# Optimization experiments

Measured on AMD Instinct MI355X. Metric: run time of the kernel, lower is better.

## Reference

```python
import jax, jax.numpy as jnp
import numpy as np

B, S, H = 2, 1024, 2048
NH, HD = 16, 128
PAST = 1024
ROPE_THETA = 10000.0


def _rope(q, k, theta=ROPE_THETA):
    # q, k: [B, S, NH, HD]; standard rotate-half RoPE over current positions 0..S-1
    s, d = q.shape[1], q.shape[3]
    inv_freq = 1.0 / (theta ** (jnp.arange(0, d, 2, dtype=jnp.float32) / d))  # [d/2]
    freqs = jnp.arange(s, dtype=jnp.float32)[:, None] * inv_freq[None, :]      # [S, d/2]
    emb = jnp.concatenate([freqs, freqs], axis=-1)                             # [S, d]
    cos = jnp.cos(emb)[None, :, None, :]
    sin = jnp.sin(emb)[None, :, None, :]

    def rot_half(x):
        x1, x2 = jnp.split(x, 2, axis=-1)
        return jnp.concatenate([-x2, x1], axis=-1)

    return q * cos + rot_half(q) * sin, k * cos + rot_half(k) * sin


def setup_inputs() -> dict:
    key = jax.random.key(0)
    ks = jax.random.split(key, 12)
    hidden_states = jax.random.normal(ks[0], (B, S, H), dtype=jnp.float32)
    past_key = jax.random.normal(ks[1], (B, NH, PAST, HD), dtype=jnp.float32)
    past_value = jax.random.normal(ks[2], (B, NH, PAST, HD), dtype=jnp.float32)
    # causal mask accounting for cache: 1.0 where masked (query i cannot see kv j > PAST+i)
    q_pos = PAST + jnp.arange(S)[:, None]
    kv_pos = jnp.arange(PAST + S)[None, :]
    mask = jnp.broadcast_to((kv_pos > q_pos).astype(jnp.float32)[None, None], (B, 1, S, PAST + S))
    sc = 1.0 / np.sqrt(H)
    Wq = jax.random.normal(ks[3], (H, NH * HD), dtype=jnp.float32) * sc
    Wk = jax.random.normal(ks[4], (H, NH * HD), dtype=jnp.float32) * sc
    Wv = jax.random.normal(ks[5], (H, NH * HD), dtype=jnp.float32) * sc
    Wo = jax.random.normal(ks[6], (NH * HD, H), dtype=jnp.float32) * (1.0 / np.sqrt(NH * HD))
    bq = jnp.zeros((NH * HD,), jnp.float32)
    bk = jnp.zeros((NH * HD,), jnp.float32)
    bv = jnp.zeros((NH * HD,), jnp.float32)
    bo = jnp.zeros((H,), jnp.float32)
    return {"hidden_states": hidden_states, "mask": mask, "past_key": past_key,
            "past_value": past_value, "Wq": Wq, "bq": bq, "Wk": Wk, "bk": bk,
            "Wv": Wv, "bv": bv, "Wo": Wo, "bo": bo}


def reference(hidden_states, mask, past_key, past_value, Wq, bq, Wk, bk, Wv, bv, Wo, bo):
    b, s, _ = hidden_states.shape
    scale = 1.0 / jnp.sqrt(jnp.float32(HD))
    q = (hidden_states @ Wq + bq).reshape(b, s, NH, HD)
    k = (hidden_states @ Wk + bk).reshape(b, s, NH, HD)
    v = (hidden_states @ Wv + bv).reshape(b, s, NH, HD)
    q, k = _rope(q, k)
    q, k, v = (jnp.transpose(x, (0, 2, 1, 3)) for x in (q, k, v))  # [B,NH,S,HD]
    k = jnp.concatenate([past_key, k], axis=2)    # [B,NH,S_total,HD]
    v = jnp.concatenate([past_value, v], axis=2)
    scores = jnp.einsum('bhqd,bhkd->bhqk', q, k) * scale
    scores = scores + mask * (-1e9)               # mask broadcasts over heads
    probs = jax.nn.softmax(scores, axis=-1).astype(jnp.float32)
    out = jnp.einsum('bhqk,bhkd->bhqd', probs, v)
    out = out.transpose(0, 2, 1, 3).reshape(b, s, NH * HD)
    return out @ Wo + bo, k, v
```

## Files before the change

### kernel.cpp

```cpp
#include <hip/hip_runtime.h>
#include <hip/hip_bf16.h>
#include <math.h>

#define NB 2
#define SEQ 1024
#define HDIM 2048
#define NHEADS 16
#define HDHEAD 128
#define PASTN 1024
#define STOT 2048
#define MROWS 2048

typedef __attribute__((ext_vector_type(4))) float f32x4;
typedef __attribute__((ext_vector_type(8))) __bf16 bf16x8;
typedef __attribute__((ext_vector_type(8))) unsigned short us8;
typedef __attribute__((ext_vector_type(4))) unsigned short us4;

__device__ __forceinline__ unsigned short f2bf(float f) {
    union { float f; unsigned int u; } v; v.f = f;
    unsigned int u = v.u;
    u += 0x7FFFu + ((u >> 16) & 1u);
    return (unsigned short)(u >> 16);
}
__device__ __forceinline__ bf16x8 as_bf(us8 u) { return __builtin_bit_cast(bf16x8, u); }

__device__ __forceinline__ void gl16(const unsigned short* g, unsigned short* l) {
    __builtin_amdgcn_global_load_lds(
        (const __attribute__((address_space(1))) void*)g,
        (__attribute__((address_space(3))) void*)l, 16, 0, 0);
}

#define OFF_CS  ((size_t)0)
#define OFF_HSB (OFF_CS  + (size_t)SEQ*64*8)
#define OFF_WT  (OFF_HSB + (size_t)MROWS*HDIM*2)
#define OFF_QBF (OFF_WT  + (size_t)4*HDIM*HDIM*2)
#define OFF_KC  (OFF_QBF + (size_t)NB*NHEADS*SEQ*HDHEAD*2)
#define OFF_VT  (OFF_KC  + (size_t)NB*NHEADS*STOT*HDHEAD*2)
#define OFF_ATT (OFF_VT  + (size_t)NB*NHEADS*HDHEAD*STOT*2)


__global__ void k_prep(const float* __restrict__ in, unsigned short* __restrict__ hsb,
                       const float* __restrict__ pk, float* __restrict__ outK,
                       unsigned short* __restrict__ Kc2, float2* __restrict__ csT,
                       const float* __restrict__ Wq, const float* __restrict__ Wk,
                       const float* __restrict__ Wv, const float* __restrict__ Wo,
                       unsigned short* __restrict__ WT,
                       const float* __restrict__ pv, float* __restrict__ outV,
                       unsigned short* __restrict__ Vt2) {
    __shared__ unsigned short tsh[64][65];
    const int bid = blockIdx.x, tid = threadIdx.x;
    if (bid < 4096) {
        const int i = (bid * 256 + tid) * 4;
        {
            f32x4 v = *(const f32x4*)(in + i);
            us4 o;
            o.x = f2bf(v.x); o.y = f2bf(v.y); o.z = f2bf(v.z); o.w = f2bf(v.w);
            *(us4*)(hsb + i) = o;
        }
        {
            size_t e = (size_t)i;
            size_t bh = e >> 17;
            int p = (int)((e >> 7) & 1023);
            int d0 = (int)(e & 127);
            f32x4 v = *(const f32x4*)(pk + e);
            *(f32x4*)(outK + e + (bh << 17)) = v;
            us4 u;
            u.x = f2bf(v.x); u.y = f2bf(v.y); u.z = f2bf(v.z); u.w = f2bf(v.w);
            const int kt = p >> 6, pr = p & 63;
            *(us4*)(Kc2 + ((bh * 32 + kt) << 13) + (size_t)pr * 128 + (d0 ^ ((p & 7) << 3))) = u;
        }
        if (bid < 256) {
            const int idx = bid * 256 + tid;
            const int s = idx >> 6, fi = idx & 63;
            float inv = 1.0f / powf(10000.0f, (float)fi / 64.0f);
            float a = (float)s * inv;
            csT[idx] = make_float2(cosf(a), sinf(a));
        }
    } else if (bid < 8192) {
        const int idx = bid - 4096;
        const int z = idx >> 10;
        const int rem = idx & 1023;
        const int n0 = (rem & 31) * 64, k0 = (rem >> 5) * 64;
        const float* W = (z == 0) ? Wq : (z == 1) ? Wk : (z == 2) ? Wv : Wo;
        unsigned short* out = WT + (size_t)z * HDIM * HDIM;
        const int tx = tid & 63, ty = tid >> 6;
        #pragma unroll
        for (int j = 0; j < 16; ++j) {
            const int kk = ty + j * 4;
            tsh[tx][kk] = f2bf(W[(size_t)(k0 + kk) * HDIM + n0 + tx]);
        }
        __syncthreads();
        #pragma unroll
        for (int j = 0; j < 16; ++j) {
            const int nn = ty + j * 4;
            out[(size_t)(n0 + nn) * HDIM + k0 + tx] = tsh[nn][tx];
        }
    } else {
        const int idx = bid - 8192;
        const int bh = idx >> 5;
        const int rem = idx & 31;
        const int p0 = (rem & 15) * 64, d0 = (rem >> 4) * 64;
        const int tx = tid & 63, ty = tid >> 6;
        const float* src = pv + ((size_t)bh * PASTN + p0) * HDHEAD + d0;
        float* dst = outV + ((size_t)bh * STOT + p0) * HDHEAD + d0;
        #pragma unroll
        for (int j = 0; j < 16; ++j) {
            const int pp = ty + j * 4;
            float v = src[(size_t)pp * HDHEAD + tx];
            dst[(size_t)pp * HDHEAD + tx] = v;
            tsh[tx][pp] = f2bf(v);
        }
        __syncthreads();
        unsigned short* vt = Vt2 + (((size_t)bh * 32 + (p0 >> 6)) << 13);
        #pragma unroll
        for (int j = 0; j < 16; ++j) {
            const int dd = ty + j * 4;
            const int d = d0 + dd;
            vt[(size_t)d * 64 + (tx ^ ((d & 7) << 3))] = tsh[dd][tx];
        }
    }
}

__global__ __launch_bounds__(512, 2) void k_gemm_qkv(
    const unsigned short* __restrict__ hsb, const unsigned short* __restrict__ WT,
    const float* __restrict__ bv,
    float* __restrict__ Cq, float* __restrict__ Ck, float* __restrict__ outV) {
    __shared__ __align__(16) unsigned short As[2][256 * 64];
    __shared__ __align__(16) unsigned short Bs[2][256 * 64];

    const int bid = blockIdx.x;
    const int swz = (bid & 7) * 24 + (bid >> 3);
    const int mb = swz & 7;
    const int nbz = swz >> 3;
    const int z = nbz >> 3;
    const int nb8 = nbz & 7;
    const int m0 = mb * 256;
    const int n0 = nb8 * 256;
    const unsigned short* Wz = WT + (size_t)z * HDIM * HDIM;

    const int t = threadIdx.x;
    const int lane = t & 63, wid = t >> 6;
    const int wr = wid >> 1, wc = wid & 1;
    const int c = lane & 15, g = lane >> 4;

    const int lrow8 = lane >> 3;
    const int lslot = (lane & 7) ^ lrow8;
    const unsigned short* aB = hsb + (size_t)(m0 + lrow8) * HDIM + lslot * 8;
    const unsigned short* bB = Wz + (size_t)(n0 + lrow8) * HDIM + lslot * 8;

    auto stage = [&](int kt, int pb) {
        const int k0s = kt * 64;
        #pragma unroll
        for (int j = 0; j < 4; ++j) {
            const int ch = wid * 4 + j;
            gl16(aB + (size_t)(ch * 8) * HDIM + k0s, &As[pb][ch * 512]);
            gl16(bB + (size_t)(ch * 8) * HDIM + k0s, &Bs[pb][ch * 512]);
        }
    };

    f32x4 acc[4][8] = {};
    const int NT = HDIM / 64;

    stage(0, 0);
    stage(1, 1);

#define MF(A_, B_, C_) __builtin_amdgcn_mfma_f32_16x16x32_bf16(A_, B_, C_, 0, 0, 0)
#define RDA(D0, D1, MI) { const int ar_ = wr * 64 + (MI) * 16 + c; const int sa_ = ar_ & 7; \
    D0 = as_bf(*(const us8*)&As[p][ar_ * 64 + ((g ^ sa_) << 3)]); \
    D1 = as_bf(*(const us8*)&As[p][ar_ * 64 + (((4 + g) ^ sa_) << 3)]); }
#define RDB0(NI) { const int br_ = wc * 128 + (NI) * 16 + c; const int sb_ = br_ & 7; \
    b0[NI] = as_bf(*(const us8*)&Bs[p][br_ * 64 + ((g ^ sb_) << 3)]); }
#define RDB1(NI) { const int br_ = wc * 128 + (NI) * 16 + c; const int sb_ = br_ & 7; \
    b1[NI] = as_bf(*(const us8*)&Bs[p][br_ * 64 + (((4 + g) ^ sb_) << 3)]); }

    for (int kt = 0; kt < NT; ++kt) {
        const int p = kt & 1;
        if (kt + 1 < NT) {
            asm volatile("s_waitcnt vmcnt(8)" ::: "memory");
        } else {
            asm volatile("s_waitcnt vmcnt(0)" ::: "memory");
        }
        __builtin_amdgcn_s_barrier();

        bf16x8 b0[8], b1[8];
        bf16x8 a0c, a1c, a0n, a1n;
        RDA(a0c, a1c, 0)
        RDB0(0) RDB0(1) RDB0(2) RDB0(3)
        __builtin_amdgcn_s_setprio(1);
        RDB0(4) acc[0][0] = MF(a0c, b0[0], acc[0][0]);
        RDB0(5) acc[0][1] = MF(a0c, b0[1], acc[0][1]);
        RDB0(6) acc[0][2] = MF(a0c, b0[2], acc[0][2]);
        RDB0(7) acc[0][3] = MF(a0c, b0[3], acc[0][3]);
        RDB1(0) acc[0][4] = MF(a0c, b0[4], acc[0][4]);
        RDB1(1) acc[0][5] = MF(a0c, b0[5], acc[0][5]);
        RDB1(2) acc[0][6] = MF(a0c, b0[6], acc[0][6]);
        RDB1(3) acc[0][7] = MF(a0c, b0[7], acc[0][7]);
        RDB1(4) acc[0][0] = MF(a1c, b1[0], acc[0][0]);
        RDB1(5) acc[0][1] = MF(a1c, b1[1], acc[0][1]);
        RDB1(6) acc[0][2] = MF(a1c, b1[2], acc[0][2]);
        RDB1(7) acc[0][3] = MF(a1c, b1[3], acc[0][3]);
        RDA(a0n, a1n, 1)
        acc[0][4] = MF(a1c, b1[4], acc[0][4]);
        acc[0][5] = MF(a1c, b1[5], acc[0][5]);
        acc[0][6] = MF(a1c, b1[6], acc[0][6]);
        acc[0][7] = MF(a1c, b1[7], acc[0][7]);
        acc[1][0] = MF(a0n, b0[0], acc[1][0]);
        acc[1][1] = MF(a0n, b0[1], acc[1][1]);
        acc[1][2] = MF(a0n, b0[2], acc[1][2]);
        acc[1][3] = MF(a0n, b0[3], acc[1][3]);
        acc[1][4] = MF(a0n, b0[4], acc[1][4]);
        acc[1][5] = MF(a0n, b0[5], acc[1][5]);
        acc[1][6] = MF(a0n, b0[6], acc[1][6]);
        acc[1][7] = MF(a0n, b0[7], acc[1][7]);
        RDA(a0c, a1c, 2)
        acc[1][0] = MF(a1n, b1[0], acc[1][0]);
        acc[1][1] = MF(a1n, b1[1], acc[1][1]);
        acc[1][2] = MF(a1n, b1[2], acc[1][2]);
        acc[1][3] = MF(a1n, b1[3], acc[1][3]);
        acc[1][4] = MF(a1n, b1[4], acc[1][4]);
        acc[1][5] = MF(a1n, b1[5], acc[1][5]);
        acc[1][6] = MF(a1n, b1[6], acc[1][6]);
        acc[1][7] = MF(a1n, b1[7], acc[1][7]);
        acc[2][0] = MF(a0c, b0[0], acc[2][0]);
        acc[2][1] = MF(a0c, b0[1], acc[2][1]);
        acc[2][2] = MF(a0c, b0[2], acc[2][2]);
        acc[2][3] = MF(a0c, b0[3], acc[2][3]);
        acc[2][4] = MF(a0c, b0[4], acc[2][4]);
        acc[2][5] = MF(a0c, b0[5], acc[2][5]);
        acc[2][6] = MF(a0c, b0[6], acc[2][6]);
        acc[2][7] = MF(a0c, b0[7], acc[2][7]);
        RDA(a0n, a1n, 3)
        acc[2][0] = MF(a1c, b1[0], acc[2][0]);
        acc[2][1] = MF(a1c, b1[1], acc[2][1]);
        acc[2][2] = MF(a1c, b1[2], acc[2][2]);
        acc[2][3] = MF(a1c, b1[3], acc[2][3]);
        acc[2][4] = MF(a1c, b1[4], acc[2][4]);
        acc[2][5] = MF(a1c, b1[5], acc[2][5]);
        acc[2][6] = MF(a1c, b1[6], acc[2][6]);
        acc[2][7] = MF(a1c, b1[7], acc[2][7]);
        acc[3][0] = MF(a0n, b0[0], acc[3][0]);
        acc[3][1] = MF(a0n, b0[1], acc[3][1]);
        acc[3][2] = MF(a0n, b0[2], acc[3][2]);
        acc[3][3] = MF(a0n, b0[3], acc[3][3]);
        acc[3][4] = MF(a0n, b0[4], acc[3][4]);
        acc[3][5] = MF(a0n, b0[5], acc[3][5]);
        acc[3][6] = MF(a0n, b0[6], acc[3][6]);
        acc[3][7] = MF(a0n, b0[7], acc[3][7]);
        acc[3][0] = MF(a1n, b1[0], acc[3][0]);
        acc[3][1] = MF(a1n, b1[1], acc[3][1]);
        acc[3][2] = MF(a1n, b1[2], acc[3][2]);
        acc[3][3] = MF(a1n, b1[3], acc[3][3]);
        acc[3][4] = MF(a1n, b1[4], acc[3][4]);
        acc[3][5] = MF(a1n, b1[5], acc[3][5]);
        acc[3][6] = MF(a1n, b1[6], acc[3][6]);
        acc[3][7] = MF(a1n, b1[7], acc[3][7]);
        __builtin_amdgcn_s_setprio(0);
        __builtin_amdgcn_s_barrier();
        if (kt + 2 < NT) stage(kt + 2, p);
    }
#undef MF
#undef RDA
#undef RDB0
#undef RDB1

    if (z < 2) {
        float* Cz = (z == 0) ? Cq : Ck;
        #pragma unroll
        for (int mi = 0; mi < 4; ++mi) {
            #pragma unroll
            for (int r = 0; r < 4; ++r) {
                const size_t row = (size_t)(m0 + wr * 64 + mi * 16 + g * 4 + r);
                #pragma unroll
                for (int ni = 0; ni < 8; ++ni)
                    Cz[row * HDIM + n0 + wc * 128 + ni * 16 + c] = acc[mi][ni][r];
            }
        }
    } else {
        const int h = nb8 * 2 + wc;
        const int b = m0 >> 10;
        const size_t bh2 = (size_t)(b * NHEADS + h);
        float bias8[8];
        #pragma unroll
        for (int ni = 0; ni < 8; ++ni) bias8[ni] = bv[n0 + wc * 128 + ni * 16 + c];
        #pragma unroll
        for (int mi = 0; mi < 4; ++mi) {
            #pragma unroll
            for (int r = 0; r < 4; ++r) {
                const int row = m0 + wr * 64 + mi * 16 + g * 4 + r;
                const int s = row & 1023;
                const int p = PASTN + s;
                #pragma unroll
                for (int ni = 0; ni < 8; ++ni)
                    outV[(bh2 * STOT + p) * HDHEAD + ni * 16 + c] = acc[mi][ni][r] + bias8[ni];
            }
        }
    }
}

__global__ __launch_bounds__(256) void k_post(
    const float* __restrict__ Cq, const float* __restrict__ Ck,
    const float* __restrict__ outV,
    const float* __restrict__ bq, const float* __restrict__ bk,
    const float2* __restrict__ csT,
    unsigned short* __restrict__ qbf, unsigned short* __restrict__ Kc2,
    unsigned short* __restrict__ Vt2, float* __restrict__ outK) {
    __shared__ unsigned short tv[128][80];
    const int stile = blockIdx.x;
    const int bh = blockIdx.y;
    const int b = bh >> 4, h = bh & 15;
    const int tid = threadIdx.x;
    const int dq = (tid & 15) * 4;
    const int sl0 = tid >> 4;
    const int s0 = stile * 64;
    const int ktv = 16 + stile;
    const float qscale = 0.08838834764831845f * 1.44269504088896f;
    unsigned short* kc = Kc2 + (((size_t)bh * 32 + ktv) << 13);
    unsigned short* vt = Vt2 + (((size_t)bh * 32 + ktv) << 13);

    float bql[4], bqh[4], bkl[4], bkh[4];
    #pragma unroll
    for (int i = 0; i < 4; ++i) {
        bql[i] = bq[h * 128 + dq + i];      bqh[i] = bq[h * 128 + 64 + dq + i];
        bkl[i] = bk[h * 128 + dq + i];      bkh[i] = bk[h * 128 + 64 + dq + i];
    }

    #pragma unroll
    for (int ps = 0; ps < 4; ++ps) {
        const int sl = sl0 + ps * 16;
        const int s = s0 + sl;
        const size_t row = (size_t)b * 1024 + s;
        const int p = PASTN + s;
        float2 cs4[4];
        #pragma unroll
        for (int i = 0; i < 4; ++i) cs4[i] = csT[s * 64 + dq + i];
        const int swzp = (sl & 7) << 3;
        {
            const f32x4 a = *(const f32x4*)&Cq[row * HDIM + h * 128 + dq];
            const f32x4 bb = *(const f32x4*)&Cq[row * HDIM + h * 128 + dq + 64];
            us4 lo, hi;
            #pragma unroll
            for (int i = 0; i < 4; ++i) {
                const float va = a[i] + bql[i];
                const float vb = bb[i] + bqh[i];
                lo[i] = f2bf((va * cs4[i].x - vb * cs4[i].y) * qscale);
                hi[i] = f2bf((vb * cs4[i].x + va * cs4[i].y) * qscale);
            }
            unsigned short* qrow = qbf + ((size_t)bh * SEQ + s) * HDHEAD;
            *(us4*)&qrow[dq] = lo;
            *(us4*)&qrow[dq + 64] = hi;
        }
        {
            const f32x4 a = *(const f32x4*)&Ck[row * HDIM + h * 128 + dq];
            const f32x4 bb = *(const f32x4*)&Ck[row * HDIM + h * 128 + dq + 64];
            f32x4 rl, rh;
            us4 lo, hi;
            #pragma unroll
            for (int i = 0; i < 4; ++i) {
                const float va = a[i] + bkl[i];
                const float vb = bb[i] + bkh[i];
                rl[i] = va * cs4[i].x - vb * cs4[i].y;
                rh[i] = vb * cs4[i].x + va * cs4[i].y;
                lo[i] = f2bf(rl[i]);
                hi[i] = f2bf(rh[i]);
            }
            float* krow = outK + ((size_t)bh * STOT + p) * HDHEAD;
            *(f32x4*)&krow[dq] = rl;
            *(f32x4*)&krow[dq + 64] = rh;
            *(us4*)&kc[(size_t)sl * 128 + (dq ^ swzp)] = lo;
            *(us4*)&kc[(size_t)sl * 128 + ((dq + 64) ^ swzp)] = hi;
        }
        {
            const f32x4 va = *(const f32x4*)&outV[((size_t)bh * STOT + p) * HDHEAD + dq];
            const f32x4 vb = *(const f32x4*)&outV[((size_t)bh * STOT + p) * HDHEAD + dq + 64];
            #pragma unroll
            for (int i = 0; i < 4; ++i) {
                tv[dq + i][sl] = f2bf(va[i]);
                tv[dq + 64 + i][sl] = f2bf(vb[i]);
            }
        }
    }
    __syncthreads();
    const int d = tid >> 1;
    const int ph = (tid & 1) * 32;
    const int swzd = (d & 7) << 3;
    #pragma unroll
    for (int i = 0; i < 8; ++i) {
        const int pp = ph + i * 4;
        us4 u;
        u.x = tv[d][pp]; u.y = tv[d][pp + 1]; u.z = tv[d][pp + 2]; u.w = tv[d][pp + 3];
        *(us4*)&vt[(size_t)d * 64 + (pp ^ swzd)] = u;
    }
}

__global__ __launch_bounds__(256) void k_attn(
    const unsigned short* __restrict__ qbf, const unsigned short* __restrict__ Kc2,
    const unsigned short* __restrict__ Vt2, unsigned short* __restrict__ attn) {
    __shared__ __align__(16) unsigned short Ks[2][64 * 128];
    __shared__ __align__(16) unsigned short Vs[128 * 64];
    __shared__ __align__(16) unsigned short P[4][16][72];
    const int bid = blockIdx.x;
    const int bh = bid & 31;
    const int qt = bid >> 5;
    const int b = bh >> 4, h = bh & 15;
    const int t = threadIdx.x, lane = t & 63, w = t >> 6;
    const int c = lane & 15, g = lane >> 4;
    const int q0 = qt * 64 + w * 16;
    const unsigned short* Qb = qbf + ((size_t)bh * SEQ + q0) * HDHEAD;
    const unsigned short* Kbase = Kc2 + ((size_t)bh << 18);
    const unsigned short* Vbase = Vt2 + ((size_t)bh << 18);

    bf16x8 qf[4];
    #pragma unroll
    for (int kf = 0; kf < 4; ++kf)
        qf[kf] = as_bf(*(const us8*)(Qb + (size_t)c * HDHEAD + kf * 32 + g * 8));

    #pragma unroll
    for (int j = 0; j < 4; ++j) {
        const int ch = w * 4 + j;
        gl16(Kbase + ch * 512 + lane * 8, &Ks[0][ch * 512]);
    }

    f32x4 o[8] = {};
    float mrow[4] = {-1e30f, -1e30f, -1e30f, -1e30f};
    float lrow[4] = {0.f, 0.f, 0.f, 0.f};
    const int nkt = 17 + qt;
    int cur = 0;
    for (int kt = 0; kt < nkt; ++kt) {
        asm volatile("s_waitcnt vmcnt(0)" ::: "memory");
        __builtin_amdgcn_s_barrier();
        const unsigned short* Vg = Vbase + ((size_t)kt << 13);
        #pragma unroll
        for (int j = 0; j < 4; ++j) {
            const int ch = w * 4 + j;
            gl16(Vg + ch * 512 + lane * 8, &Vs[ch * 512]);
        }
        if (kt + 1 < nkt) {
            const unsigned short* Kg = Kbase + ((size_t)(kt + 1) << 13);
            #pragma unroll
            for (int j = 0; j < 4; ++j) {
                const int ch = w * 4 + j;
                gl16(Kg + ch * 512 + lane * 8, &Ks[cur ^ 1][ch * 512]);
            }
        }
        f32x4 sa[4] = {};
        #pragma unroll
        for (int nf = 0; nf < 4; ++nf) {
            const int row = nf * 16 + c;
            const int swzr = (row & 7) << 3;
            #pragma unroll
            for (int kf = 0; kf < 4; ++kf) {
                bf16x8 kf8 = as_bf(*(const us8*)&Ks[cur][row * 128 + ((kf * 32 + g * 8) ^ swzr)]);
                sa[nf] = __builtin_amdgcn_mfma_f32_16x16x32_bf16(qf[kf], kf8, sa[nf], 0, 0, 0);
            }
        }
        const int k0 = kt * 64;
        if (k0 + 63 > PASTN + q0) {
            #pragma unroll
            for (int nf = 0; nf < 4; ++nf) {
                const int j = k0 + nf * 16 + c;
                #pragma unroll
                for (int r = 0; r < 4; ++r)
                    if (j > PASTN + q0 + g * 4 + r) sa[nf][r] = -1e30f;
            }
        }
        float pmax[4];
        #pragma unroll
        for (int r = 0; r < 4; ++r)
            pmax[r] = fmaxf(fmaxf(sa[0][r], sa[1][r]), fmaxf(sa[2][r], sa[3][r]));
        bool need = false;
        #pragma unroll
        for (int r = 0; r < 4; ++r) need = need || (pmax[r] > mrow[r] + 12.0f);
        if (__any(need)) {
            #pragma unroll
            for (int r = 0; r < 4; ++r) {
                float mx = pmax[r];
                mx = fmaxf(mx, __shfl_xor(mx, 1));
                mx = fmaxf(mx, __shfl_xor(mx, 2));
                mx = fmaxf(mx, __shfl_xor(mx, 4));
                mx = fmaxf(mx, __shfl_xor(mx, 8));
                const float mnew = fmaxf(mrow[r], mx);
                const float alpha = exp2f(mrow[r] - mnew);
                mrow[r] = mnew;
                lrow[r] *= alpha;
                #pragma unroll
                for (int nd = 0; nd < 8; ++nd) o[nd][r] *= alpha;
            }
        }
        #pragma unroll
        for (int r = 0; r < 4; ++r) {
            const float p0 = exp2f(sa[0][r] - mrow[r]);
            const float p1 = exp2f(sa[1][r] - mrow[r]);
            const float p2 = exp2f(sa[2][r] - mrow[r]);
            const float p3 = exp2f(sa[3][r] - mrow[r]);
            lrow[r] += (p0 + p1) + (p2 + p3);
            P[w][g * 4 + r][0 * 16 + c] = f2bf(p0);
            P[w][g * 4 + r][1 * 16 + c] = f2bf(p1);
            P[w][g * 4 + r][2 * 16 + c] = f2bf(p2);
            P[w][g * 4 + r][3 * 16 + c] = f2bf(p3);
        }
        if (kt + 1 < nkt) {
            asm volatile("s_waitcnt vmcnt(4)" ::: "memory");
        } else {
            asm volatile("s_waitcnt vmcnt(0)" ::: "memory");
        }
        __builtin_amdgcn_s_barrier();
        #pragma unroll
        for (int kf2 = 0; kf2 < 2; ++kf2) {
            const bf16x8 pa = as_bf(*(const us8*)&P[w][c][kf2 * 32 + g * 8]);
            #pragma unroll
            for (int nd = 0; nd < 8; ++nd) {
                const int d = nd * 16 + c;
                const bf16x8 vf = as_bf(*(const us8*)&Vs[d * 64 + ((kf2 * 32 + g * 8) ^ ((d & 7) << 3))]);
                o[nd] = __builtin_amdgcn_mfma_f32_16x16x32_bf16(pa, vf, o[nd], 0, 0, 0);
            }
        }
        cur ^= 1;
    }
    #pragma unroll
    for (int r = 0; r < 4; ++r) {
        float ls = lrow[r];
        ls += __shfl_xor(ls, 1);
        ls += __shfl_xor(ls, 2);
        ls += __shfl_xor(ls, 4);
        ls += __shfl_xor(ls, 8);
        const float inv = 1.0f / ls;
        #pragma unroll
        for (int nd = 0; nd < 8; ++nd) o[nd][r] *= inv;
    }
    #pragma unroll
    for (int nd = 0; nd < 8; ++nd)
        #pragma unroll
        for (int r = 0; r < 4; ++r) {
            const int srow = q0 + g * 4 + r;
            attn[((size_t)b * SEQ + srow) * HDIM + h * HDHEAD + nd * 16 + c] = f2bf(o[nd][r]);
        }
}

__global__ __launch_bounds__(256) void k_gemm_out(
    const unsigned short* __restrict__ attn, const unsigned short* __restrict__ WTo,
    const float* __restrict__ bo, float* __restrict__ out) {
    __shared__ __align__(16) unsigned char SMEM[65536];
    unsigned short* As0 = (unsigned short*)SMEM;
    unsigned short* Bs0 = (unsigned short*)(SMEM + 32768);
    const int m0 = blockIdx.y * 128;
    const int n0 = blockIdx.x * 128;
    const int t = threadIdx.x;
    const int lane = t & 63, w = t >> 6;
    const int c = lane & 15, g = lane >> 4;

    const int lrow = lane >> 3;
    const int lslot = (lane & 7) ^ lrow;
    const unsigned short* aB = attn + (size_t)(m0 + lrow) * HDIM + lslot * 8;
    const unsigned short* bB = WTo + (size_t)(n0 + lrow) * HDIM + lslot * 8;

    f32x4 acc[2][8] = {};
    const int NT = HDIM / 64;

    #pragma unroll
    for (int j = 0; j < 4; ++j) {
        const int ch = w * 4 + j;
        gl16(aB + (size_t)(ch * 8) * HDIM, &As0[ch * 512]);
        gl16(bB + (size_t)(ch * 8) * HDIM, &Bs0[ch * 512]);
    }
    for (int kt = 0; kt < NT; ++kt) {
        const int cb = kt & 1;
        if (kt + 1 < NT) {
            const int k1 = (kt + 1) * 64;
            #pragma unroll
            for (int j = 0; j < 4; ++j) {
                const int ch = w * 4 + j;
                gl16(aB + (size_t)(ch * 8) * HDIM + k1, &As0[(cb ^ 1) * 8192 + ch * 512]);
                gl16(bB + (size_t)(ch * 8) * HDIM + k1, &Bs0[(cb ^ 1) * 8192 + ch * 512]);
            }
            asm volatile("s_waitcnt vmcnt(8)" ::: "memory");
        } else {
            asm volatile("s_waitcnt vmcnt(0)" ::: "memory");
        }
        __builtin_amdgcn_s_barrier();
        #pragma unroll
        for (int kc = 0; kc < 2; ++kc) {
            bf16x8 af[2];
            #pragma unroll
            for (int mi = 0; mi < 2; ++mi) {
                const int ar = w * 32 + mi * 16 + c;
                af[mi] = as_bf(*(const us8*)&As0[cb * 8192 + ar * 64 + (((kc * 4 + g) ^ (ar & 7)) << 3)]);
            }
            #pragma unroll
            for (int ni = 0; ni < 8; ++ni) {
                const int br = ni * 16 + c;
                bf16x8 bfrag = as_bf(*(const us8*)&Bs0[cb * 8192 + br * 64 + (((kc * 4 + g) ^ (br & 7)) << 3)]);
                acc[0][ni] = __builtin_amdgcn_mfma_f32_16x16x32_bf16(af[0], bfrag, acc[0][ni], 0, 0, 0);
                acc[1][ni] = __builtin_amdgcn_mfma_f32_16x16x32_bf16(af[1], bfrag, acc[1][ni], 0, 0, 0);
            }
        }
        __builtin_amdgcn_s_barrier();
    }

    float* myF = (float*)SMEM + w * (16 * 132);
    const int qrow = lane & 31;
    for (int mi = 0; mi < 2; ++mi) {
        __syncthreads();
        #pragma unroll
        for (int r = 0; r < 4; ++r) {
            const int row = g * 4 + r;
            #pragma unroll
            for (int ni = 0; ni < 8; ++ni)
                myF[row * 132 + ni * 16 + c] = acc[mi][ni][r];
        }
        __syncthreads();
        #pragma unroll
        for (int j = 0; j < 8; ++j) {
            const int rrow = 2 * j + (lane >> 5);
            const int row = m0 + w * 32 + mi * 16 + rrow;
            f32x4 v4 = *(const f32x4*)&myF[rrow * 132 + qrow * 4];
            const f32x4 b4 = *(const f32x4*)&bo[n0 + qrow * 4];
            v4 += b4;
            *(f32x4*)&out[(size_t)row * HDIM + n0 + qrow * 4] = v4;
        }
    }
}

extern "C" void kernel_launch(void* const* d_in, const int* in_sizes, int n_in,
                              void* d_out, int out_size, void* d_ws, size_t ws_size,
                              hipStream_t stream) {
    const float* hidden = (const float*)d_in[0];
    const float* past_key = (const float*)d_in[2];
    const float* past_value = (const float*)d_in[3];
    const float* Wq = (const float*)d_in[4];
    const float* bq = (const float*)d_in[5];
    const float* Wk = (const float*)d_in[6];
    const float* bk = (const float*)d_in[7];
    const float* Wv = (const float*)d_in[8];
    const float* bv = (const float*)d_in[9];
    const float* Wo = (const float*)d_in[10];
    const float* bo = (const float*)d_in[11];

    float* out0 = (float*)d_out;
    float* outK = out0 + (size_t)NB * SEQ * HDIM;
    float* outV = outK + (size_t)NB * NHEADS * STOT * HDHEAD;

    char* ws = (char*)d_ws;
    float2* csT = (float2*)(ws + OFF_CS);
    unsigned short* hsb = (unsigned short*)(ws + OFF_HSB);
    unsigned short* WT = (unsigned short*)(ws + OFF_WT);
    unsigned short* qbf = (unsigned short*)(ws + OFF_QBF);
    unsigned short* Kc2 = (unsigned short*)(ws + OFF_KC);
    unsigned short* Vt2 = (unsigned short*)(ws + OFF_VT);
    unsigned short* attnb = (unsigned short*)(ws + OFF_ATT);
    float* Cq = out0;
    float* Ck = (float*)(ws + OFF_ATT);

    k_prep<<<dim3(9216), dim3(256), 0, stream>>>(
        hidden, hsb, past_key, outK, Kc2, csT,
        Wq, Wk, Wv, Wo, WT, past_value, outV, Vt2);
    k_gemm_qkv<<<dim3(192), dim3(512), 0, stream>>>(
        hsb, WT, bv, Cq, Ck, outV);
    k_post<<<dim3(16, 32), dim3(256), 0, stream>>>(
        Cq, Ck, outV, bq, bk, csT, qbf, Kc2, Vt2, outK);
    k_attn<<<dim3(512), dim3(256), 0, stream>>>(qbf, Kc2, Vt2, attnb);
    k_gemm_out<<<dim3(16, 16), dim3(256), 0, stream>>>(
        attnb, WT + (size_t)3 * HDIM * HDIM, bo, out0);
}
```

Measured before the change: 216.5 us.

## Move past K/V copy and bf16 repack from prep kernel into QKV GEMM launch

The past_key/past_value copy to the output and their bf16 swizzled repacking now run in 64 extra blocks appended to the QKV GEMM grid instead of in the prep kernel. The intent is to overlap this memory-bound work with the compute-bound GEMM, since the GEMM has only 192 blocks on a 256-CU device and leaves CUs idle. The trade-off is that the extra blocks are large-LDS, 512-thread blocks that each loop over many tiles, so they may finish later than the GEMM blocks and extend the kernel's tail.

```diff
diff --git a/kernel.cpp b/kernel.cpp
--- a/kernel.cpp
+++ b/kernel.cpp
@@ -40,35 +40,18 @@
 
 
 __global__ void k_prep(const float* __restrict__ in, unsigned short* __restrict__ hsb,
-                       const float* __restrict__ pk, float* __restrict__ outK,
-                       unsigned short* __restrict__ Kc2, float2* __restrict__ csT,
+                       float2* __restrict__ csT,
                        const float* __restrict__ Wq, const float* __restrict__ Wk,
                        const float* __restrict__ Wv, const float* __restrict__ Wo,
-                       unsigned short* __restrict__ WT,
-                       const float* __restrict__ pv, float* __restrict__ outV,
-                       unsigned short* __restrict__ Vt2) {
+                       unsigned short* __restrict__ WT) {
     __shared__ unsigned short tsh[64][65];
     const int bid = blockIdx.x, tid = threadIdx.x;
     if (bid < 4096) {
         const int i = (bid * 256 + tid) * 4;
-        {
-            f32x4 v = *(const f32x4*)(in + i);
-            us4 o;
-            o.x = f2bf(v.x); o.y = f2bf(v.y); o.z = f2bf(v.z); o.w = f2bf(v.w);
-            *(us4*)(hsb + i) = o;
-        }
-        {
-            size_t e = (size_t)i;
-            size_t bh = e >> 17;
-            int p = (int)((e >> 7) & 1023);
-            int d0 = (int)(e & 127);
-            f32x4 v = *(const f32x4*)(pk + e);
-            *(f32x4*)(outK + e + (bh << 17)) = v;
-            us4 u;
-            u.x = f2bf(v.x); u.y = f2bf(v.y); u.z = f2bf(v.z); u.w = f2bf(v.w);
-            const int kt = p >> 6, pr = p & 63;
-            *(us4*)(Kc2 + ((bh * 32 + kt) << 13) + (size_t)pr * 128 + (d0 ^ ((p & 7) << 3))) = u;
-        }
+        f32x4 v = *(const f32x4*)(in + i);
+        us4 o;
+        o.x = f2bf(v.x); o.y = f2bf(v.y); o.z = f2bf(v.z); o.w = f2bf(v.w);
+        *(us4*)(hsb + i) = o;
         if (bid < 256) {
             const int idx = bid * 256 + tid;
             const int s = idx >> 6, fi = idx & 63;
@@ -76,7 +59,7 @@
             float a = (float)s * inv;
             csT[idx] = make_float2(cosf(a), sinf(a));
         }
-    } else if (bid < 8192) {
+    } else {
         const int idx = bid - 4096;
         const int z = idx >> 10;
         const int rem = idx & 1023;
@@ -95,40 +78,69 @@
             const int nn = ty + j * 4;
             out[(size_t)(n0 + nn) * HDIM + k0 + tx] = tsh[nn][tx];
         }
-    } else {
-        const int idx = bid - 8192;
-        const int bh = idx >> 5;
-        const int rem = idx & 31;
-        const int p0 = (rem & 15) * 64, d0 = (rem >> 4) * 64;
-        const int tx = tid & 63, ty = tid >> 6;
-        const float* src = pv + ((size_t)bh * PASTN + p0) * HDHEAD + d0;
-        float* dst = outV + ((size_t)bh * STOT + p0) * HDHEAD + d0;
-        #pragma unroll
-        for (int j = 0; j < 16; ++j) {
-            const int pp = ty + j * 4;
-            float v = src[(size_t)pp * HDHEAD + tx];
-            dst[(size_t)pp * HDHEAD + tx] = v;
-            tsh[tx][pp] = f2bf(v);
-        }
-        __syncthreads();
-        unsigned short* vt = Vt2 + (((size_t)bh * 32 + (p0 >> 6)) << 13);
-        #pragma unroll
-        for (int j = 0; j < 16; ++j) {
-            const int dd = ty + j * 4;
-            const int d = d0 + dd;
-            vt[(size_t)d * 64 + (tx ^ ((d & 7) << 3))] = tsh[dd][tx];
-        }
     }
 }
 
 __global__ __launch_bounds__(512, 2) void k_gemm_qkv(
     const unsigned short* __restrict__ hsb, const unsigned short* __restrict__ WT,
     const float* __restrict__ bv,
-    float* __restrict__ Cq, float* __restrict__ Ck, float* __restrict__ outV) {
+    float* __restrict__ Cq, float* __restrict__ Ck, float* __restrict__ outV,
+    const float* __restrict__ pk, const float* __restrict__ pv,
+    float* __restrict__ outK, unsigned short* __restrict__ Kc2,
+    unsigned short* __restrict__ Vt2) {
     __shared__ __align__(16) unsigned short As[2][256 * 64];
     __shared__ __align__(16) unsigned short Bs[2][256 * 64];
 
     const int bid = blockIdx.x;
+    const int t = threadIdx.x;
+
+    if (bid >= 192) {
+        if (bid < 224) {
+            const int blk = bid - 192;
+            for (int it = 0; it < 64; ++it) {
+                const size_t e = ((size_t)(blk * 64 + it) * 512 + t) * 4;
+                const size_t bh = e >> 17;
+                const int p = (int)((e >> 7) & 1023);
+                const int d0 = (int)(e & 127);
+                f32x4 v = *(const f32x4*)(pk + e);
+                *(f32x4*)(outK + e + (bh << 17)) = v;
+                us4 u;
+                u.x = f2bf(v.x); u.y = f2bf(v.y); u.z = f2bf(v.z); u.w = f2bf(v.w);
+                *(us4*)(Kc2 + ((bh * 32 + (p >> 6)) << 13) + (size_t)(p & 63) * 128 +
+                        (d0 ^ ((p & 7) << 3))) = u;
+            }
+        } else {
+            const int blk = bid - 224;
+            unsigned short (*tsh)[65] = (unsigned short (*)[65])As;
+            const int tx = t & 63, ty = t >> 6;
+            for (int tt = 0; tt < 32; ++tt) {
+                const int tile = blk * 32 + tt;
+                const int bh = tile >> 5;
+                const int rem = tile & 31;
+                const int p0 = (rem & 15) * 64, d0 = (rem >> 4) * 64;
+                const float* src = pv + ((size_t)bh * PASTN + p0) * HDHEAD + d0;
+                float* dst = outV + ((size_t)bh * STOT + p0) * HDHEAD + d0;
+                #pragma unroll
+                for (int j = 0; j < 8; ++j) {
+                    const int pp = ty + j * 8;
+                    float v = src[(size_t)pp * HDHEAD + tx];
+                    dst[(size_t)pp * HDHEAD + tx] = v;
+                    tsh[tx][pp] = f2bf(v);
+                }
+                __syncthreads();
+                unsigned short* vt = Vt2 + (((size_t)bh * 32 + (p0 >> 6)) << 13);
+                #pragma unroll
+                for (int j = 0; j < 8; ++j) {
+                    const int dd = ty + j * 8;
+                    const int d = d0 + dd;
+                    vt[(size_t)d * 64 + (tx ^ ((d & 7) << 3))] = tsh[dd][tx];
+                }
+                __syncthreads();
+            }
+        }
+        return;
+    }
+
     const int swz = (bid & 7) * 24 + (bid >> 3);
     const int mb = swz & 7;
     const int nbz = swz >> 3;
@@ -138,7 +150,6 @@
     const int n0 = nb8 * 256;
     const unsigned short* Wz = WT + (size_t)z * HDIM * HDIM;
 
-    const int t = threadIdx.x;
     const int lane = t & 63, wid = t >> 6;
     const int wr = wid >> 1, wc = wid & 1;
     const int c = lane & 15, g = lane >> 4;
@@ -650,11 +661,10 @@
     float* Cq = out0;
     float* Ck = (float*)(ws + OFF_ATT);
 
-    k_prep<<<dim3(9216), dim3(256), 0, stream>>>(
-        hidden, hsb, past_key, outK, Kc2, csT,
-        Wq, Wk, Wv, Wo, WT, past_value, outV, Vt2);
-    k_gemm_qkv<<<dim3(192), dim3(512), 0, stream>>>(
-        hsb, WT, bv, Cq, Ck, outV);
+    k_prep<<<dim3(8192), dim3(256), 0, stream>>>(
+        hidden, hsb, csT, Wq, Wk, Wv, Wo, WT);
+    k_gemm_qkv<<<dim3(256), dim3(512), 0, stream>>>(
+        hsb, WT, bv, Cq, Ck, outV, past_key, past_value, outK, Kc2, Vt2);
     k_post<<<dim3(16, 32), dim3(256), 0, stream>>>(
         Cq, Ck, outV, bq, bk, csT, qbf, Kc2, Vt2, outK);
     k_attn<<<dim3(512), dim3(256), 0, stream>>>(qbf, Kc2, Vt2, attnb);
```

Measured after the change: 205.5 us. -5.1%, faster.
